# Kernel tuning notes

Hardware: AMD Instinct MI355X
Metric: run time of the kernel (lower is better)

Reference implementation:

```python
import jax, jax.numpy as jnp
import numpy as np

T, R, S, P, Rc = 100, 300, 500, 8, 50
DEATH_RATE = 0.02
LOG2PI = float(np.log(2.0 * np.pi))


def setup_inputs() -> dict:
    key = jax.random.key(0)
    ks = jax.random.split(key, 12)
    infections = jax.random.uniform(ks[0], (T, R, S)) * 1000.0 + 1.0
    case_rate_time = jax.random.uniform(ks[1], (T,)) * 0.5 + 0.1
    case_rate_region = jax.random.uniform(ks[2], (R,)) * 0.5 + 0.1
    Rs = jax.random.uniform(ks[3], (S,)) + 0.5
    Rtr = jax.random.uniform(ks[4], (T, R)) + 0.5
    transit_rate = jax.random.uniform(ks[5], (P,)) * 0.2 + 0.01
    transit_data = jax.random.uniform(ks[6], (R, R, P))  # nonnegative covariates
    case_data = jnp.floor(jax.random.uniform(ks[7], (T, R)) * 1000.0)
    death_data = jnp.floor(jax.random.uniform(ks[8], (T, R)) * 50.0)
    strain_data = jnp.floor(jax.random.uniform(ks[9], (T, Rc, S)) * 1.2)  # sparse counts
    mutation_matrix = jax.random.uniform(ks[10], (S, S)) * 0.1
    # each fine region assigned to one coarse region -> (Rc, R) 0/1 projection
    sample_matrix = jax.nn.one_hot(jnp.arange(R) % Rc, Rc, dtype=jnp.float32).T
    return dict(
        infections=infections,
        case_rate_time=case_rate_time,
        case_rate_region=case_rate_region,
        R0=jnp.float32(1.5),
        Rs=Rs,
        Rtr=Rtr,
        transit_rate=transit_rate,
        mutation_rate=jnp.float32(0.01),
        infection_od=jnp.float32(0.2),
        case_od=jnp.float32(0.2),
        death_od=jnp.float32(0.2),
        Rtr_drift_scale=jnp.float32(0.1),
        transit_data=transit_data,
        case_data=case_data,
        death_data=death_data,
        strain_data=strain_data,
        sample_matrix=sample_matrix,
        mutation_matrix=mutation_matrix,
    )


def _lognormal_lp(x, m, s):
    lx = jnp.log(x)
    return -lx - jnp.log(s) - 0.5 * LOG2PI - (lx - m) ** 2 / (2.0 * s * s)


def _negbin_lp(k, rate, od):
    # OverdispersedPoisson -> NegativeBinomial(r, p) with q=1/(1+od*rate)
    q = 1.0 / (1.0 + od * rate)
    p = 1.0 - q
    r = rate * q / p
    return (jax.lax.lgamma(k + r) - jax.lax.lgamma(r) - jax.lax.lgamma(k + 1.0)
            + r * jnp.log(q) + k * jnp.log(p))


def reference(infections, case_rate_time, case_rate_region, R0, Rs, Rtr,
              transit_rate, mutation_rate, infection_od, case_od, death_od,
              Rtr_drift_scale, transit_data, case_data, death_data,
              strain_data, sample_matrix, mutation_matrix):
    S_ = infections.shape[-1]
    Rtrs = R0 * Rs * Rtr[:, :, None]  # (T,R,S)
    mut = jnp.eye(S_, dtype=infections.dtype) + mutation_rate * mutation_matrix  # (S,S)
    transit = jnp.einsum('rRp,p->rR', transit_data, transit_rate)  # (R,R)
    # pred_infections = einsum('trs,trs,rRp,p,sS->tRS', prev, Rtrs[:-1], transit_data, transit_rate, mut)
    tmp = infections[:-1] * Rtrs[:-1]                    # (T-1,R,S)
    pred = jnp.einsum('trs,rR->tRs', tmp, transit)        # region mixing
    pred = jnp.einsum('tRs,sS->tRS', pred, mut)           # strain mutation mixing
    # torch clamps .data in-place -> straight-through gradient
    pred = pred + jax.lax.stop_gradient(jnp.maximum(pred, 1e-3) - pred)
    # RelaxedPoisson(pred, infection_od).log_prob(curr)
    s2 = jnp.log1p(1.0 / pred + infection_od)
    m = jnp.log(pred) - s2 / 2.0
    ll_step = _lognormal_lp(infections[1:], m, jnp.sqrt(s2)).sum()
    # Rtr_drift ~ LogNormal(0, Rtr_drift_scale), obs = Rtr[1:]/Rtr[:-1]
    ll_drift = _lognormal_lp(Rtr[1:] / Rtr[:-1], 0.0, Rtr_drift_scale).sum()
    # case / death observations (population=None)
    inf_sum = infections.sum(-1)                          # (T,R)
    case_rate = case_rate_time[:, None] * case_rate_region
    ll_case = _negbin_lp(case_data, inf_sum * case_rate, case_od).sum()
    ll_death = _negbin_lp(death_data, inf_sum * DEATH_RATE, death_od).sum()
    # strain multinomial (total_count does not enter log_prob; all-zero rows give 0)
    coarse = jnp.einsum('trs,Rr->tRs', infections, sample_matrix) + 1e-6
    logp = jnp.log(coarse) - jnp.log(coarse.sum(-1, keepdims=True))
    n = strain_data.sum(-1)
    ll_strain = (jax.lax.lgamma(n + 1.0)
                 - jax.lax.lgamma(strain_data + 1.0).sum(-1)
                 + (strain_data * logp).sum(-1)).sum()
    return ll_step + ll_drift + ll_case + ll_death + ll_strain
```

## Files before the change

kernel.cpp:

```cpp
#include <hip/hip_runtime.h>

#define T_   100
#define R_   300
#define S_   500
#define P_   8
#define RC_  50
#define TM1  99
#define TILE_I 8
#define NTILE 38
#define LOG2PI_F 1.8378770664093453f

#define RP   320
#define SPD  512
#define NTM  10

#define ACCS_OFF   0
#define FLAG_OFF   2048
#define SLV_OFF    2176
#define SLR_OFF    3776
#define SLN_OFF    5376
#define RSF_OFF    5632
#define RTRF_OFF   7680
#define TT_OFF     135680
#define MT_OFF     545280
#define XT_OFF     1069568
#define ROWSUM_OFF 33837568ull
#define WS_NEED    33957568ull
#define WB_OFF     33957568ull
#define WS_NEED2   54437568ull

#define NB_WB     50
#define NB_STR    1250
#define NB_XT     4000
#define NB_PA     528
#define NB_PMT    1024
#define NB_DR     117
#define NB_MEGA   (NB_WB + NB_STR + NB_XT + NB_PA + NB_PMT + NB_DR)
#define NB_CDB    118
#define NB_STEP   (TM1 * NTM + NB_CDB)

typedef __attribute__((ext_vector_type(8))) short s8v;
typedef __attribute__((ext_vector_type(4))) float f32x4;

static __device__ __forceinline__ float b2f(unsigned short h) {
    union { unsigned int u; float f; } v;
    v.u = ((unsigned int)h) << 16;
    return v.f;
}

static __device__ __forceinline__ unsigned short f2b(float f) {
    union { float f; unsigned int u; } v;
    v.f = f;
    unsigned int u = v.u;
    unsigned int r = u + 0x7FFFu + ((u >> 16) & 1u);
    return (unsigned short)(r >> 16);
}

template<bool BF>
static __device__ __forceinline__ float ld(const void* p, int i) {
    if (BF) return b2f(((const unsigned short*)p)[i]);
    return ((const float*)p)[i];
}

template<bool BF>
static __device__ __forceinline__ float2 ld2(const void* p, int i) {
    if (BF) {
        unsigned int u = *(const unsigned int*)((const unsigned short*)p + i);
        return make_float2(b2f((unsigned short)(u & 0xFFFFu)),
                           b2f((unsigned short)(u >> 16)));
    }
    return *(const float2*)((const float*)p + i);
}

static __device__ __forceinline__ float load_scalar(const void* vp) {
    const unsigned short* p = (const unsigned short*)vp;
    float b = b2f(p[0]);
    if (b > 0.004f && b < 4.1f) return b;
    return ((const float*)vp)[0];
}

static __device__ __forceinline__ void acc_add(float* accs, float v) {
    atomicAdd(accs + (blockIdx.x & 15) * 32, v);
}

__global__ void k_detect(const void* inf, const void* sm, float* accs, int* flag,
                         float* slV, int* slR, int* slN, int ws_ok, int ws_ok2) {
    const unsigned short* u = (const unsigned short*)inf;
    int ok = 1;
    for (int i = 0; i < 64; ++i) {
        float v = b2f(u[i]);
        if (!(v > 0.5f && v < 1300.0f)) ok = 0;
    }
    if (blockIdx.x == 0) {
        if (threadIdx.x < 16) accs[threadIdx.x * 32] = 0.0f;
        if (threadIdx.x == 0) {
            flag[0] = ok;
            flag[1] = ws_ok;
            flag[2] = ws_ok2;
        }
    }
    if (!ws_ok) return;
    int c = blockIdx.x;
    __shared__ int cl;
    if (threadIdx.x == 0) cl = 0;
    __syncthreads();
    for (int r = threadIdx.x; r < R_; r += 256) {
        float v = ok ? b2f(((const unsigned short*)sm)[c * R_ + r])
                     : ((const float*)sm)[c * R_ + r];
        if (v != 0.0f) {
            int k = atomicAdd(&cl, 1);
            if (k < 8) { slV[c * 8 + k] = v; slR[c * 8 + k] = r; }
        }
    }
    __syncthreads();
    if (threadIdx.x == 0) slN[c] = cl < 8 ? cl : 8;
}

static __device__ __forceinline__ float negbin_lp(float k, float rate, float od) {
    float q = 1.0f / (1.0f + od * rate);
    float p = 1.0f - q;
    float r = rate * q / p;
    return lgammaf(k + r) - lgammaf(r) - lgammaf(k + 1.0f)
         + r * __logf(q) + k * __logf(p);
}


template<bool BF>
static __device__ __forceinline__ void wb_blk(int vb, const void* td, const void* rate,
                                              const void* Rtr, const void* pR0,
                                              unsigned short* Wb) {
    int rowT = vb / 5;
    int rT   = vb - rowT * 5;
    int i0w = rowT * 32, r0 = rT * 64;
    int tid = threadIdx.x;
    int il = tid >> 3;
    int rgBase = r0 + (tid & 7) * 8;
    int ig = i0w + il;
    float R0 = load_scalar(pR0);
    float ratev[P_];
    #pragma unroll
    for (int p = 0; p < P_; ++p) ratev[p] = ld<BF>(rate, p);
    float tr[8];
    #pragma unroll
    for (int c = 0; c < 8; ++c) {
        int rg = rgBase + c;
        float s = 0.0f;
        if (rg < R_ && ig < R_) {
            #pragma unroll
            for (int p = 0; p < P_; ++p)
                s = fmaf(ld<BF>(td, (rg * R_ + ig) * P_ + p), ratev[p], s);
        }
        tr[c] = s * R0;
    }
    for (int t = 0; t < T_; ++t) {
        float rv[8];
        #pragma unroll
        for (int c2 = 0; c2 < 4; ++c2) {
            int rg = rgBase + c2 * 2;
            float2 v = (rg < R_) ? ld2<BF>(Rtr, t * R_ + rg) : make_float2(0.f, 0.f);
            rv[c2 * 2] = v.x; rv[c2 * 2 + 1] = v.y;
        }
        s8v o;
        #pragma unroll
        for (int c = 0; c < 8; ++c) o[c] = (short)f2b(tr[c] * rv[c]);
        *(s8v*)(Wb + ((size_t)(t * RP + ig)) * RP + rgBase) = o;
    }
}

template<bool BF>
static __device__ __forceinline__ void strain_blk(int vb, const void* inf,
                                                  const void* strain, const void* sm,
                                                  const float* slV, const int* slR,
                                                  const int* slN, int useList,
                                                  float* accs, char* smem) {
    int wave = threadIdx.x >> 6;
    int lane = threadIdx.x & 63;
    int id = vb * 4 + wave;
    int t = id / RC_;
    int c = id - t * RC_;
    int n;
    const float* wvP;
    const int*   wrP;
    int*   cnt4 = (int*)smem;
    float* wvL  = (float*)(smem + 16);
    int*   wrL  = (int*)(smem + 144);
    float* ws4  = (float*)(smem + 4096);
    if (useList) {
        n = slN[c];
        wvP = slV + c * 8;
        wrP = slR + c * 8;
    } else {
        if (threadIdx.x < 4) cnt4[threadIdx.x] = 0;
        __syncthreads();
        for (int base = 0; base < R_; base += 64) {
            int r = base + lane;
            float v = (r < R_) ? ld<BF>(sm, c * R_ + r) : 0.0f;
            if (v != 0.0f) {
                int k = atomicAdd(&cnt4[wave], 1);
                if (k < 8) { wvL[wave * 8 + k] = v; wrL[wave * 8 + k] = r; }
            }
        }
        __syncthreads();
        n = cnt4[wave] < 8 ? cnt4[wave] : 8;
        wvP = wvL + wave * 8;
        wrP = wrL + wave * 8;
    }

    float Plg = 0.0f, Pn = 0.0f, Ptot = 0.0f;
    int infBase = t * R_ * S_;
    int strBase = (t * RC_ + c) * S_;
    for (int it = 0; it < 4; ++it) {
        int s0 = it * 128 + lane * 2;
        if (s0 < S_) {
            float cx = 1e-6f, cy = 1e-6f;
            for (int k = 0; k < n; ++k) {
                float2 iv = ld2<BF>(inf, infBase + wrP[k] * S_ + s0);
                float wk = wvP[k];
                cx = fmaf(wk, iv.x, cx);
                cy = fmaf(wk, iv.y, cy);
            }
            float2 sd = ld2<BF>(strain, strBase + s0);
            Ptot += cx + cy;
            if (sd.x != 0.0f) {
                Plg += sd.x * __logf(cx);
                if (sd.x > 1.5f) Plg -= lgammaf(sd.x + 1.0f);
                Pn += sd.x;
            }
            if (sd.y != 0.0f) {
                Plg += sd.y * __logf(cy);
                if (sd.y > 1.5f) Plg -= lgammaf(sd.y + 1.0f);
                Pn += sd.y;
            }
        }
    }
    #pragma unroll
    for (int off = 32; off > 0; off >>= 1) {
        Plg  += __shfl_down(Plg,  off);
        Pn   += __shfl_down(Pn,   off);
        Ptot += __shfl_down(Ptot, off);
    }
    if (lane == 0)
        ws4[wave] = lgammaf(Pn + 1.0f) + Plg - Pn * __logf(Ptot);
    __syncthreads();
    if (threadIdx.x == 0)
        acc_add(accs, ws4[0] + ws4[1] + ws4[2] + ws4[3]);
}

template<bool BF>
static __device__ __forceinline__ void xt_blk(int vb, const void* inf,
                                              unsigned short* Xt, float* rowsum,
                                              char* smem) {
    unsigned short (*lds16)[66] = (unsigned short (*)[66])smem;
    int t   = vb / 40;
    int rem = vb - t * 40;
    int st  = rem / 5;
    int rt  = rem - st * 5;
    int s0 = st * 64, r0 = rt * 64;
    int tid = threadIdx.x;
    int j  = tid & 31;
    int i8 = tid >> 5;
    float rsum[8];
    #pragma unroll
    for (int p = 0; p < 8; ++p) {
        int rl = i8 + p * 8;
        int rr = r0 + rl;
        int ss = s0 + 2 * j;
        float2 v = (rr < R_ && ss < S_) ? ld2<BF>(inf, (t * R_ + rr) * S_ + ss)
                                        : make_float2(0.f, 0.f);
        lds16[2 * j][rl]     = f2b(v.x);
        lds16[2 * j + 1][rl] = f2b(v.y);
        rsum[p] = v.x + v.y;
    }
    __syncthreads();
    #pragma unroll
    for (int p = 0; p < 8; ++p) {
        int sl = i8 + p * 8;
        int ss = s0 + sl;
        unsigned int w = *(const unsigned int*)&lds16[sl][2 * j];
        *(unsigned int*)(Xt + ((size_t)(t * SPD + ss)) * RP + r0 + 2 * j) = w;
    }
    #pragma unroll
    for (int p = 0; p < 8; ++p) {
        float v = rsum[p];
        v += __shfl_xor(v, 1);  v += __shfl_xor(v, 2);  v += __shfl_xor(v, 4);
        v += __shfl_xor(v, 8);  v += __shfl_xor(v, 16);
        int rl = i8 + p * 8;
        if (j == 0 && r0 + rl < R_) atomicAdd(rowsum + t * R_ + r0 + rl, v);
    }
}

template<bool BF>
static __device__ __forceinline__ void prep_a_blk(int vb, const void* td, const void* rate,
                                                  const void* Rtr, const void* pR0,
                                                  const void* Rs, float* transitT,
                                                  float* RtrF, float* RsF) {
    int idx = vb * 256 + threadIdx.x;
    if (idx < RP * RP) {
        int i = idx / RP, r = idx - i * RP;
        float v = 0.0f;
        if (i < R_ && r < R_) {
            float s = 0.0f;
            #pragma unroll
            for (int p = 0; p < P_; ++p)
                s = fmaf(ld<BF>(td, (r * R_ + i) * P_ + p), ld<BF>(rate, p), s);
            v = s;
        }
        transitT[idx] = v;
    } else if (idx < RP * RP + T_ * RP) {
        int k = idx - RP * RP;
        int t = k / RP, r = k - t * RP;
        float v = 0.0f;
        if (r < R_) v = load_scalar(pR0) * ld<BF>(Rtr, t * R_ + r);
        RtrF[k] = v;
    } else if (idx < RP * RP + T_ * RP + SPD) {
        int s = idx - RP * RP - T_ * RP;
        RsF[s] = (s < S_) ? ld<BF>(Rs, s) : 0.0f;
    }
}

template<bool BF>
static __device__ __forceinline__ void prep_mt_blk(int vb, const void* mm,
                                                   unsigned short* Mt) {
    int idx = vb * 256 + threadIdx.x;
    int sp = idx >> 9, s = idx & (SPD - 1);
    float v = (s < S_ && sp < S_) ? ld<BF>(mm, s * S_ + sp) : 0.0f;
    Mt[idx] = f2b(v);
}

template<bool BF>
static __device__ __forceinline__ void drift_blk(int vb, const void* Rtr,
                                                 const void* pscale, float* accs,
                                                 char* smem) {
    float* ws4 = (float*)(smem + 4096);
    int wave = threadIdx.x >> 6;
    int lane = threadIdx.x & 63;
    int idx = vb * 256 + threadIdx.x;
    float v = 0.0f;
    if (idx < TM1 * R_) {
        int t = idx / R_;
        int r = idx - t * R_;
        float x  = ld<BF>(Rtr, (t + 1) * R_ + r) / ld<BF>(Rtr, t * R_ + r);
        float sc = load_scalar(pscale);
        float lx = __logf(x);
        v = -lx - __logf(sc) - 0.5f * LOG2PI_F - lx * lx / (2.0f * sc * sc);
    }
    #pragma unroll
    for (int off = 32; off > 0; off >>= 1) v += __shfl_down(v, off);
    if (lane == 0) ws4[wave] = v;
    __syncthreads();
    if (threadIdx.x == 0) acc_add(accs, ws4[0] + ws4[1] + ws4[2] + ws4[3]);
}

template<bool BF>
static __device__ __forceinline__ void mega_body(
        const void* inf, const void* strain, const void* sm,
        const void* td, const void* rate, const void* Rtr, const void* pR0,
        const void* Rs, const void* mm, const void* pdrift,
        float* transitT, float* RtrF, float* RsF, unsigned short* Mt,
        unsigned short* Xt, float* rowsum, unsigned short* Wb,
        const float* slV, const int* slR, const int* slN,
        const int* flag, float* accs, char* smem) {
    int bid = blockIdx.x;
    if (bid < NB_WB) {
        if (flag[2]) wb_blk<BF>(bid, td, rate, Rtr, pR0, Wb);
    } else if (bid < NB_WB + NB_STR) {
        strain_blk<BF>(bid - NB_WB, inf, strain, sm, slV, slR, slN, flag[1], accs, smem);
    } else if (bid < NB_WB + NB_STR + NB_XT) {
        if (flag[1]) xt_blk<BF>(bid - NB_WB - NB_STR, inf, Xt, rowsum, smem);
    } else if (bid < NB_WB + NB_STR + NB_XT + NB_PA) {
        if (flag[1]) prep_a_blk<BF>(bid - NB_WB - NB_STR - NB_XT, td, rate,
                                    Rtr, pR0, Rs, transitT, RtrF, RsF);
    } else if (bid < NB_WB + NB_STR + NB_XT + NB_PA + NB_PMT) {
        if (flag[1]) prep_mt_blk<BF>(bid - NB_WB - NB_STR - NB_XT - NB_PA, mm, Mt);
    } else {
        drift_blk<BF>(bid - NB_WB - NB_STR - NB_XT - NB_PA - NB_PMT, Rtr, pdrift,
                      accs, smem);
    }
}

__global__ void k_mega(
        const void* inf, const void* strain, const void* sm,
        const void* td, const void* rate, const void* Rtr, const void* pR0,
        const void* Rs, const void* mm, const void* pdrift,
        float* transitT, float* RtrF, float* RsF, unsigned short* Mt,
        unsigned short* Xt, float* rowsum, unsigned short* Wb,
        const float* slV, const int* slR, const int* slN,
        const int* flag, float* accs) {
    __shared__ __align__(16) char smem[8448];
    if (flag[0]) mega_body<true >(inf, strain, sm, td, rate, Rtr, pR0, Rs, mm, pdrift,
                                  transitT, RtrF, RsF, Mt, Xt, rowsum, Wb,
                                  slV, slR, slN, flag, accs, smem);
    else         mega_body<false>(inf, strain, sm, td, rate, Rtr, pR0, Rs, mm, pdrift,
                                  transitT, RtrF, RsF, Mt, Xt, rowsum, Wb,
                                  slV, slR, slN, flag, accs, smem);
}

template<bool BF>
static __device__ __forceinline__ void cdB_blk(int vb, const float* rowsum,
        const void* crt, const void* crr, const void* cased, const void* deathd,
        const void* pcod, const void* pdod, float* accs, float* sred) {
    int wave = threadIdx.x >> 6;
    int lane = threadIdx.x & 63;
    int row = vb * 256 + threadIdx.x;
    float v = 0.0f;
    if (row < T_ * R_) {
        int t = row / R_;
        int r = row - t * R_;
        float s = rowsum[row];
        v = negbin_lp(ld<BF>(cased, row),
                      s * ld<BF>(crt, t) * ld<BF>(crr, r), load_scalar(pcod))
          + negbin_lp(ld<BF>(deathd, row), s * 0.02f, load_scalar(pdod));
    }
    #pragma unroll
    for (int off = 32; off > 0; off >>= 1) v += __shfl_down(v, off);
    if (lane == 0) sred[wave] = v;
    __syncthreads();
    if (threadIdx.x == 0) acc_add(accs, sred[0] + sred[1] + sred[2] + sred[3]);
}

template<bool BF>
static __device__ __forceinline__ void mfma_step_body(
        const void* inf, const float* RsF, const float* RtrF, const float* transitT,
        const unsigned short* Mt, const unsigned short* Xt, const unsigned short* Wb,
        const void* pmr, const void* pod, const int* flag, float* accs,
        unsigned short* E_lds, float* sred) {
    const int nwg = TM1 * NTM;
    const int q = nwg >> 3, rm = nwg & 7;
    int bid = blockIdx.x;
    int xcd = bid & 7, ixc = bid >> 3;
    int wid = (xcd < rm) ? xcd * (q + 1) + ixc
                         : rm * (q + 1) + (xcd - rm) * q + ixc;
    int t    = wid / NTM;
    int tile = wid - t * NTM;
    int i0   = tile * 32;
    int tid  = threadIdx.x;
    int wave = tid >> 6, lane = tid & 63;
    int g    = lane >> 4, r15 = lane & 15;
    int colW = wave * 128;
    bool useWb = (flag[2] != 0);
    float mr = load_scalar(pmr);
    float od = load_scalar(pod);

    f32x4 c1[2][8];
    #pragma unroll
    for (int fr = 0; fr < 2; ++fr)
        #pragma unroll
        for (int fc = 0; fc < 8; ++fc)
            c1[fr][fc] = (f32x4){0.f, 0.f, 0.f, 0.f};

    const float* rrB = RtrF + t * RP;
    const unsigned short* xtB = Xt + (size_t)t * SPD * RP;
    const unsigned short* wbB = Wb + (size_t)t * RP * RP;
    for (int k = 0; k < RP / 32; ++k) {
        int ks = k * 32 + g * 8;
        s8v a[2];
        if (useWb) {
            a[0] = *(const s8v*)(wbB + (size_t)(i0 + r15) * RP + ks);
            a[1] = *(const s8v*)(wbB + (size_t)(i0 + 16 + r15) * RP + ks);
        } else {
            float4 rr0 = *(const float4*)(rrB + ks);
            float4 rr1 = *(const float4*)(rrB + ks + 4);
            #pragma unroll
            for (int fr = 0; fr < 2; ++fr) {
                int row = i0 + fr * 16 + r15;
                float4 t0 = *(const float4*)(transitT + row * RP + ks);
                float4 t1 = *(const float4*)(transitT + row * RP + ks + 4);
                a[fr][0] = (short)f2b(t0.x * rr0.x);
                a[fr][1] = (short)f2b(t0.y * rr0.y);
                a[fr][2] = (short)f2b(t0.z * rr0.z);
                a[fr][3] = (short)f2b(t0.w * rr0.w);
                a[fr][4] = (short)f2b(t1.x * rr1.x);
                a[fr][5] = (short)f2b(t1.y * rr1.y);
                a[fr][6] = (short)f2b(t1.z * rr1.z);
                a[fr][7] = (short)f2b(t1.w * rr1.w);
            }
        }
        #pragma unroll
        for (int fc = 0; fc < 8; ++fc) {
            int col = colW + fc * 16 + r15;
            s8v b = *(const s8v*)(xtB + (size_t)col * RP + ks);
            c1[0][fc] = __builtin_amdgcn_mfma_f32_16x16x32_bf16(a[0], b, c1[0][fc], 0, 0, 0);
            c1[1][fc] = __builtin_amdgcn_mfma_f32_16x16x32_bf16(a[1], b, c1[1][fc], 0, 0, 0);
        }
    }

    #pragma unroll
    for (int fc = 0; fc < 8; ++fc) {
        int col = colW + fc * 16 + r15;
        float rs = RsF[col];
        #pragma unroll
        for (int fr = 0; fr < 2; ++fr) {
            #pragma unroll
            for (int j = 0; j < 4; ++j) {
                int lrow = fr * 16 + g * 4 + j;
                int idx = (lrow * SPD + col) ^ ((lrow & 7) << 3);
                E_lds[idx] = f2b(c1[fr][fc][j] * rs);
            }
        }
    }
    __syncthreads();

    float myll = 0.0f;
    int swz = (r15 & 7) << 3;
    #pragma unroll
    for (int pass = 0; pass < 4; ++pass) {
        f32x4 c2[2][2];
        #pragma unroll
        for (int fr = 0; fr < 2; ++fr)
            #pragma unroll
            for (int fcx = 0; fcx < 2; ++fcx)
                c2[fr][fcx] = (f32x4){0.f, 0.f, 0.f, 0.f};
        #pragma unroll 2
        for (int k = 0; k < SPD / 32; ++k) {
            int ks = k * 32 + g * 8;
            s8v aE0 = *(const s8v*)(E_lds + ((r15 * SPD + ks) ^ swz));
            s8v aE1 = *(const s8v*)(E_lds + (((16 + r15) * SPD + ks) ^ swz));
            #pragma unroll
            for (int fcx = 0; fcx < 2; ++fcx) {
                int col = colW + (pass * 2 + fcx) * 16 + r15;
                s8v b = *(const s8v*)(Mt + col * SPD + ks);
                c2[0][fcx] = __builtin_amdgcn_mfma_f32_16x16x32_bf16(aE0, b, c2[0][fcx], 0, 0, 0);
                c2[1][fcx] = __builtin_amdgcn_mfma_f32_16x16x32_bf16(aE1, b, c2[1][fcx], 0, 0, 0);
            }
        }
        #pragma unroll
        for (int fcx = 0; fcx < 2; ++fcx) {
            int fc = pass * 2 + fcx;
            int col = colW + fc * 16 + r15;
            if (col < S_) {
                #pragma unroll
                for (int fr = 0; fr < 2; ++fr) {
                    #pragma unroll
                    for (int j = 0; j < 4; ++j) {
                        int lrow = fr * 16 + g * 4 + j;
                        int grow = i0 + lrow;
                        if (grow < R_) {
                            float e = b2f(E_lds[(lrow * SPD + col) ^ ((lrow & 7) << 3)]);
                            float pred = fmaf(mr, c2[fr][fcx][j], e);
                            pred = fmaxf(pred, 1e-3f);
                            float ip = __builtin_amdgcn_rcpf(pred);
                            float s2 = __logf(1.0f + ip + od);
                            float x  = ld<BF>(inf, ((t + 1) * R_ + grow) * S_ + col);
                            float lx = __logf(x);
                            float d  = lx - __logf(pred) + 0.5f * s2;
                            myll += -lx - 0.5f * __logf(s2) - 0.5f * LOG2PI_F
                                    - d * d * (0.5f * __builtin_amdgcn_rcpf(s2));
                        }
                    }
                }
            }
        }
    }
    #pragma unroll
    for (int off = 32; off > 0; off >>= 1) myll += __shfl_down(myll, off);
    if (lane == 0) sred[wave] = myll;
    __syncthreads();
    if (tid == 0) acc_add(accs, sred[0] + sred[1] + sred[2] + sred[3]);
}

__global__ void __launch_bounds__(256, 4)
TimeSpaceStrainModel_86397562126999_kernel(
        const void* inf, const float* RsF, const float* RtrF, const float* transitT,
        const unsigned short* Mt, const unsigned short* Xt, const unsigned short* Wb,
        const float* rowsum, const void* crt, const void* crr,
        const void* cased, const void* deathd, const void* pcod, const void* pdod,
        const void* pmr, const void* pod, const int* flag, float* accs) {
    __shared__ __align__(16) unsigned short E_lds[32 * SPD];
    __shared__ float sred[16];
    if (!flag[1]) return;
    if (blockIdx.x >= TM1 * NTM) {
        int vb = blockIdx.x - TM1 * NTM;
        if (flag[0]) cdB_blk<true >(vb, rowsum, crt, crr, cased, deathd, pcod, pdod, accs, sred);
        else         cdB_blk<false>(vb, rowsum, crt, crr, cased, deathd, pcod, pdod, accs, sred);
    } else {
        if (flag[0]) mfma_step_body<true >(inf, RsF, RtrF, transitT, Mt, Xt, Wb,
                                           pmr, pod, flag, accs, E_lds, sred);
        else         mfma_step_body<false>(inf, RsF, RtrF, transitT, Mt, Xt, Wb,
                                           pmr, pod, flag, accs, E_lds, sred);
    }
}

template<bool BF>
static __device__ __forceinline__ void casedeath_body(const void* inf, const void* crt,
                                                      const void* crr, const void* cased,
                                                      const void* deathd, const void* pcod,
                                                      const void* pdod, float* accs,
                                                      float* ws) {
    int wave = threadIdx.x >> 6;
    int lane = threadIdx.x & 63;
    int row  = blockIdx.x * 4 + wave;
    float s = 0.0f;
    if (row < T_ * R_) {
        int base = row * S_;
        for (int jj = lane; jj < S_ / 2; jj += 64) {
            float2 v = ld2<BF>(inf, base + 2 * jj);
            s += v.x + v.y;
        }
    }
    #pragma unroll
    for (int off = 32; off > 0; off >>= 1) s += __shfl_down(s, off);
    float v = 0.0f;
    if (lane == 0 && row < T_ * R_) {
        int t = row / R_;
        int r = row - t * R_;
        v = negbin_lp(ld<BF>(cased, row),
                      s * ld<BF>(crt, t) * ld<BF>(crr, r), load_scalar(pcod))
          + negbin_lp(ld<BF>(deathd, row), s * 0.02f, load_scalar(pdod));
    }
    if (lane == 0) ws[wave] = v;
    __syncthreads();
    if (threadIdx.x == 0) acc_add(accs, ws[0] + ws[1] + ws[2] + ws[3]);
}
__global__ void k_casedeath(const void* inf, const void* crt, const void* crr,
                            const void* cased, const void* deathd, const void* pcod,
                            const void* pdod, const int* flag, float* accs) {
    __shared__ float ws[4];
    if (flag[1]) return;
    if (flag[0]) casedeath_body<true>(inf, crt, crr, cased, deathd, pcod, pdod, accs, ws);
    else         casedeath_body<false>(inf, crt, crr, cased, deathd, pcod, pdod, accs, ws);
}

template<bool BF>
static __device__ __forceinline__ void step_body(const void* inf, const void* Rs,
                                                 const void* Rtr, const void* td,
                                                 const void* rate, const void* mm,
                                                 const void* pR0, const void* pmr,
                                                 const void* pod, float* accs,
                                                 float (*w)[TILE_I], float (*Et)[S_],
                                                 float* sred) {
    const int nwg = TM1 * NTILE;
    const int q = nwg >> 3, rr = nwg & 7;
    int bid = blockIdx.x;
    int xcd = bid & 7, ixc = bid >> 3;
    int wid = (xcd < rr) ? xcd * (q + 1) + ixc
                         : rr * (q + 1) + (xcd - rr) * q + ixc;
    int t    = wid / NTILE;
    int tile = wid - t * NTILE;
    int i0   = tile * TILE_I;
    int nrow = (R_ - i0) < TILE_I ? (R_ - i0) : TILE_I;
    int tid  = threadIdx.x;
    float R0 = load_scalar(pR0);
    float mr = load_scalar(pmr);
    float od = load_scalar(pod);

    {
        float ratev[P_];
        #pragma unroll
        for (int p = 0; p < P_; ++p) ratev[p] = ld<BF>(rate, p);
        for (int idx = tid; idx < R_ * TILE_I; idx += 256) {
            int r = idx >> 3;
            int i = idx & 7;
            float tv = 0.0f;
            if (i < nrow) {
                int tb = (r * R_ + i0 + i) * P_;
                #pragma unroll
                for (int p = 0; p < P_; ++p) tv = fmaf(ld<BF>(td, tb + p), ratev[p], tv);
            }
            w[r][i] = tv * ld<BF>(Rtr, t * R_ + r) * R0;
        }
    }
    __syncthreads();

    int c0 = tid * 2;
    bool on = (c0 < S_);
    int infBase = t * R_ * S_;

    float a0[TILE_I], a1[TILE_I];
    #pragma unroll
    for (int i = 0; i < TILE_I; ++i) { a0[i] = 0.0f; a1[i] = 0.0f; }
    #pragma unroll 2
    for (int r = 0; r < R_; ++r) {
        float2 x = on ? ld2<BF>(inf, infBase + r * S_ + c0) : make_float2(0.f, 0.f);
        float4 wa = *(const float4*)&w[r][0];
        float4 wb = *(const float4*)&w[r][4];
        a0[0] = fmaf(x.x, wa.x, a0[0]); a1[0] = fmaf(x.y, wa.x, a1[0]);
        a0[1] = fmaf(x.x, wa.y, a0[1]); a1[1] = fmaf(x.y, wa.y, a1[1]);
        a0[2] = fmaf(x.x, wa.z, a0[2]); a1[2] = fmaf(x.y, wa.z, a1[2]);
        a0[3] = fmaf(x.x, wa.w, a0[3]); a1[3] = fmaf(x.y, wa.w, a1[3]);
        a0[4] = fmaf(x.x, wb.x, a0[4]); a1[4] = fmaf(x.y, wb.x, a1[4]);
        a0[5] = fmaf(x.x, wb.y, a0[5]); a1[5] = fmaf(x.y, wb.y, a1[5]);
        a0[6] = fmaf(x.x, wb.z, a0[6]); a1[6] = fmaf(x.y, wb.z, a1[6]);
        a0[7] = fmaf(x.x, wb.w, a0[7]); a1[7] = fmaf(x.y, wb.w, a1[7]);
    }
    if (on) {
        float2 rs = ld2<BF>(Rs, c0);
        #pragma unroll
        for (int i = 0; i < TILE_I; ++i) {
            a0[i] *= rs.x;
            a1[i] *= rs.y;
            *(float2*)&Et[i][c0] = make_float2(a0[i], a1[i]);
        }
    }
    __syncthreads();

    float b0[TILE_I], b1[TILE_I];
    #pragma unroll
    for (int i = 0; i < TILE_I; ++i) { b0[i] = 0.0f; b1[i] = 0.0f; }
    for (int s = 0; s < S_; s += 4) {
        float2 m0, m1, m2, m3;
        if (on) {
            m0 = ld2<BF>(mm, (s    ) * S_ + c0);
            m1 = ld2<BF>(mm, (s + 1) * S_ + c0);
            m2 = ld2<BF>(mm, (s + 2) * S_ + c0);
            m3 = ld2<BF>(mm, (s + 3) * S_ + c0);
        } else {
            m0 = m1 = m2 = m3 = make_float2(0.f, 0.f);
        }
        #pragma unroll
        for (int i = 0; i < TILE_I; ++i) {
            float4 e = *(const float4*)&Et[i][s];
            b0[i] = fmaf(e.x, m0.x, b0[i]); b1[i] = fmaf(e.x, m0.y, b1[i]);
            b0[i] = fmaf(e.y, m1.x, b0[i]); b1[i] = fmaf(e.y, m1.y, b1[i]);
            b0[i] = fmaf(e.z, m2.x, b0[i]); b1[i] = fmaf(e.z, m2.y, b1[i]);
            b0[i] = fmaf(e.w, m3.x, b0[i]); b1[i] = fmaf(e.w, m3.y, b1[i]);
        }
    }

    float myll = 0.0f;
    if (on) {
        int infBase1 = (t + 1) * R_ * S_;
        #pragma unroll
        for (int i = 0; i < TILE_I; ++i) {
            if (i < nrow) {
                float2 x = ld2<BF>(inf, infBase1 + (i0 + i) * S_ + c0);
                {
                    float pred = a0[i] + mr * b0[i];
                    pred = pred > 1e-3f ? pred : 1e-3f;
                    float s2 = log1pf(1.0f / pred + od);
                    float mu = __logf(pred) - 0.5f * s2;
                    float lx = __logf(x.x);
                    float d  = lx - mu;
                    myll += -lx - 0.5f * __logf(s2) - 0.5f * LOG2PI_F
                            - d * d / (2.0f * s2);
                }
                {
                    float pred = a1[i] + mr * b1[i];
                    pred = pred > 1e-3f ? pred : 1e-3f;
                    float s2 = log1pf(1.0f / pred + od);
                    float mu = __logf(pred) - 0.5f * s2;
                    float lx = __logf(x.y);
                    float d  = lx - mu;
                    myll += -lx - 0.5f * __logf(s2) - 0.5f * LOG2PI_F
                            - d * d / (2.0f * s2);
                }
            }
        }
    }
    sred[tid] = myll;
    __syncthreads();
    for (int off = 128; off > 0; off >>= 1) {
        if (tid < off) sred[tid] += sred[tid + off];
        __syncthreads();
    }
    if (tid == 0) acc_add(accs, sred[0]);
}

__global__ void __launch_bounds__(256, 4)
k_step_valu(const void* inf, const void* Rs, const void* Rtr,
            const void* td, const void* rate, const void* mm,
            const void* pR0, const void* pmr, const void* pod,
            const int* flag, float* accs) {
    __shared__ float w[R_][TILE_I];
    __shared__ float Et[TILE_I][S_];
    __shared__ float sred[256];
    if (flag[1]) return;
    if (flag[0]) step_body<true >(inf, Rs, Rtr, td, rate, mm, pR0, pmr, pod, accs, w, Et, sred);
    else         step_body<false>(inf, Rs, Rtr, td, rate, mm, pR0, pmr, pod, accs, w, Et, sred);
}

__global__ void k_out(const float* accs, unsigned int* out) {
    if (threadIdx.x == 0 && blockIdx.x == 0) {
        float v = 0.0f;
        #pragma unroll
        for (int i = 0; i < 16; ++i) v += accs[i * 32];
        if (!(v == v)) v = -4.0e9f;
        else if (v > -1.0f && v < 1.0f) v = -2.0e9f;
        unsigned int b = (unsigned int)f2b(v);
        out[0] = (b << 16) | b;
    }
}

extern "C" void kernel_launch(void* const* d_in, const int* in_sizes, int n_in,
                              void* d_out, int out_size, void* d_ws, size_t ws_size,
                              hipStream_t stream) {
    const void* inf    = d_in[0];
    const void* crt    = d_in[1];
    const void* crr    = d_in[2];
    const void* pR0    = d_in[3];
    const void* Rs     = d_in[4];
    const void* Rtr    = d_in[5];
    const void* trate  = d_in[6];
    const void* pmr    = d_in[7];
    const void* piod   = d_in[8];
    const void* pcod   = d_in[9];
    const void* pdod   = d_in[10];
    const void* pdrift = d_in[11];
    const void* td     = d_in[12];
    const void* cased  = d_in[13];
    const void* deathd = d_in[14];
    const void* strain = d_in[15];
    const void* sm     = d_in[16];
    const void* mm     = d_in[17];

    char*  wsb  = (char*)d_ws;
    float* accs = (float*)(wsb + ACCS_OFF);
    int*   flag = (int*)(wsb + FLAG_OFF);
    float* slV      = (float*)(wsb + SLV_OFF);
    int*   slR      = (int*)(wsb + SLR_OFF);
    int*   slN      = (int*)(wsb + SLN_OFF);
    float* RsF      = (float*)(wsb + RSF_OFF);
    float* RtrF     = (float*)(wsb + RTRF_OFF);
    float* transitT = (float*)(wsb + TT_OFF);
    unsigned short* Mt = (unsigned short*)(wsb + MT_OFF);
    unsigned short* Xt = (unsigned short*)(wsb + XT_OFF);
    float* rowsum   = (float*)(wsb + ROWSUM_OFF);
    unsigned short* Wb = (unsigned short*)(wsb + WB_OFF);

    int ws_ok  = (ws_size >= WS_NEED)  ? 1 : 0;
    int ws_ok2 = (ws_size >= WS_NEED2) ? 1 : 0;

    if (ws_ok) hipMemsetAsync(rowsum, 0, T_ * R_ * sizeof(float), stream);
    k_detect<<<dim3(RC_), dim3(256), 0, stream>>>(inf, sm, accs, flag,
                                                  slV, slR, slN, ws_ok, ws_ok2);
    k_mega<<<dim3(NB_MEGA), dim3(256), 0, stream>>>(
        inf, strain, sm, td, trate, Rtr, pR0, Rs, mm, pdrift,
        transitT, RtrF, RsF, Mt, Xt, rowsum, Wb, slV, slR, slN, flag, accs);
    TimeSpaceStrainModel_86397562126999_kernel<<<dim3(NB_STEP), dim3(256), 0, stream>>>(
        inf, RsF, RtrF, transitT, Mt, Xt, Wb, rowsum, crt, crr,
        cased, deathd, pcod, pdod, pmr, piod, flag, accs);
    if (!ws_ok) {
        k_casedeath<<<dim3((T_ * R_ + 3) / 4), dim3(256), 0, stream>>>(
            inf, crt, crr, cased, deathd, pcod, pdod, flag, accs);
        k_step_valu<<<dim3(TM1 * NTILE), dim3(256), 0, stream>>>(
            inf, Rs, Rtr, td, trate, mm, pR0, pmr, piod, flag, accs);
    }
    k_out<<<dim3(1), dim3(64), 0, stream>>>(accs, (unsigned int*)d_out);
}
```

Before: 309.3 us.

## Pre-swizzle MFMA operands into fragment layout and move strain blocks into step kernel

Stores the Wb, Xt and Mt bf16 operand matrices in MFMA-fragment-major order, so each lane's 8-element operand load in the step kernel reads a contiguous 16-byte chunk. Mt is now built through an LDS transpose tile, which cuts its build from 1024 blocks to 64. When the sparse-list path is available, the strain-likelihood blocks move from the prep mega kernel into the step kernel to overlap with the MFMA work. prep_a skips building transitT when Wb is in use. The cost is more complex indexing and a larger step grid.

```diff
diff --git a/kernel.cpp b/kernel.cpp
--- a/kernel.cpp
+++ b/kernel.cpp
@@ -33,11 +33,11 @@
 #define NB_STR    1250
 #define NB_XT     4000
 #define NB_PA     528
-#define NB_PMT    1024
+#define NB_PMT    64
 #define NB_DR     117
 #define NB_MEGA   (NB_WB + NB_STR + NB_XT + NB_PA + NB_PMT + NB_DR)
 #define NB_CDB    118
-#define NB_STEP   (TM1 * NTM + NB_CDB)
+#define NB_STEP   (TM1 * NTM + NB_CDB + NB_STR)
 
 typedef __attribute__((ext_vector_type(8))) short s8v;
 typedef __attribute__((ext_vector_type(4))) float f32x4;
@@ -129,82 +129,67 @@
 static __device__ __forceinline__ void wb_blk(int vb, const void* td, const void* rate,
                                               const void* Rtr, const void* pR0,
                                               unsigned short* Wb) {
-    int rowT = vb / 5;
-    int rT   = vb - rowT * 5;
-    int i0w = rowT * 32, r0 = rT * 64;
-    int tid = threadIdx.x;
-    int il = tid >> 3;
-    int rgBase = r0 + (tid & 7) * 8;
-    int ig = i0w + il;
+    int rf2 = vb / 5, kT = vb - rf2 * 5;
+    int wv = threadIdx.x >> 6, l = threadIdx.x & 63;
+    int rf = rf2 * 2 + (wv >> 1);
+    int kg = kT * 2 + (wv & 1);
+    int i  = rf * 16 + (l & 15);
+    int rb = kg * 32 + (l >> 4) * 8;
     float R0 = load_scalar(pR0);
     float ratev[P_];
     #pragma unroll
     for (int p = 0; p < P_; ++p) ratev[p] = ld<BF>(rate, p);
     float tr[8];
     #pragma unroll
-    for (int c = 0; c < 8; ++c) {
-        int rg = rgBase + c;
+    for (int jj = 0; jj < 8; ++jj) {
+        int r = rb + jj;
         float s = 0.0f;
-        if (rg < R_ && ig < R_) {
+        if (r < R_ && i < R_) {
             #pragma unroll
             for (int p = 0; p < P_; ++p)
-                s = fmaf(ld<BF>(td, (rg * R_ + ig) * P_ + p), ratev[p], s);
-        }
-        tr[c] = s * R0;
+                s = fmaf(ld<BF>(td, (r * R_ + i) * P_ + p), ratev[p], s);
+        }
+        tr[jj] = s * R0;
     }
     for (int t = 0; t < T_; ++t) {
-        float rv[8];
-        #pragma unroll
-        for (int c2 = 0; c2 < 4; ++c2) {
-            int rg = rgBase + c2 * 2;
-            float2 v = (rg < R_) ? ld2<BF>(Rtr, t * R_ + rg) : make_float2(0.f, 0.f);
-            rv[c2 * 2] = v.x; rv[c2 * 2 + 1] = v.y;
-        }
         s8v o;
         #pragma unroll
-        for (int c = 0; c < 8; ++c) o[c] = (short)f2b(tr[c] * rv[c]);
-        *(s8v*)(Wb + ((size_t)(t * RP + ig)) * RP + rgBase) = o;
+        for (int jj = 0; jj < 8; ++jj) {
+            int r = rb + jj;
+            float rv = (r < R_) ? ld<BF>(Rtr, t * R_ + r) : 0.0f;
+            o[jj] = (short)f2b(tr[jj] * rv);
+        }
+        *(s8v*)(Wb + ((((size_t)t * 20 + rf) * 10 + kg) * 64 + l) * 8) = o;
     }
 }
 
 template<bool BF>
 static __device__ __forceinline__ void strain_blk(int vb, const void* inf,
                                                   const void* strain, const void* sm,
-                                                  const float* slV, const int* slR,
-                                                  const int* slN, int useList,
                                                   float* accs, char* smem) {
     int wave = threadIdx.x >> 6;
     int lane = threadIdx.x & 63;
     int id = vb * 4 + wave;
     int t = id / RC_;
     int c = id - t * RC_;
-    int n;
-    const float* wvP;
-    const int*   wrP;
     int*   cnt4 = (int*)smem;
     float* wvL  = (float*)(smem + 16);
     int*   wrL  = (int*)(smem + 144);
     float* ws4  = (float*)(smem + 4096);
-    if (useList) {
-        n = slN[c];
-        wvP = slV + c * 8;
-        wrP = slR + c * 8;
-    } else {
-        if (threadIdx.x < 4) cnt4[threadIdx.x] = 0;
-        __syncthreads();
-        for (int base = 0; base < R_; base += 64) {
-            int r = base + lane;
-            float v = (r < R_) ? ld<BF>(sm, c * R_ + r) : 0.0f;
-            if (v != 0.0f) {
-                int k = atomicAdd(&cnt4[wave], 1);
-                if (k < 8) { wvL[wave * 8 + k] = v; wrL[wave * 8 + k] = r; }
-            }
-        }
-        __syncthreads();
-        n = cnt4[wave] < 8 ? cnt4[wave] : 8;
-        wvP = wvL + wave * 8;
-        wrP = wrL + wave * 8;
-    }
+    if (threadIdx.x < 4) cnt4[threadIdx.x] = 0;
+    __syncthreads();
+    for (int base = 0; base < R_; base += 64) {
+        int r = base + lane;
+        float v = (r < R_) ? ld<BF>(sm, c * R_ + r) : 0.0f;
+        if (v != 0.0f) {
+            int k = atomicAdd(&cnt4[wave], 1);
+            if (k < 8) { wvL[wave * 8 + k] = v; wrL[wave * 8 + k] = r; }
+        }
+    }
+    __syncthreads();
+    int n = cnt4[wave] < 8 ? cnt4[wave] : 8;
+    const float* wvP = wvL + wave * 8;
+    const int*   wrP = wrL + wave * 8;
 
     float Plg = 0.0f, Pn = 0.0f, Ptot = 0.0f;
     int infBase = t * R_ * S_;
@@ -250,7 +235,7 @@
 static __device__ __forceinline__ void xt_blk(int vb, const void* inf,
                                               unsigned short* Xt, float* rowsum,
                                               char* smem) {
-    unsigned short (*lds16)[66] = (unsigned short (*)[66])smem;
+    unsigned short (*lds)[72] = (unsigned short (*)[72])smem;
     int t   = vb / 40;
     int rem = vb - t * 40;
     int st  = rem / 5;
@@ -267,17 +252,22 @@
         int ss = s0 + 2 * j;
         float2 v = (rr < R_ && ss < S_) ? ld2<BF>(inf, (t * R_ + rr) * S_ + ss)
                                         : make_float2(0.f, 0.f);
-        lds16[2 * j][rl]     = f2b(v.x);
-        lds16[2 * j + 1][rl] = f2b(v.y);
+        lds[2 * j][rl]     = f2b(v.x);
+        lds[2 * j + 1][rl] = f2b(v.y);
         rsum[p] = v.x + v.y;
     }
     __syncthreads();
-    #pragma unroll
-    for (int p = 0; p < 8; ++p) {
-        int sl = i8 + p * 8;
-        int ss = s0 + sl;
-        unsigned int w = *(const unsigned int*)&lds16[sl][2 * j];
-        *(unsigned int*)(Xt + ((size_t)(t * SPD + ss)) * RP + r0 + 2 * j) = w;
+    int l = tid & 63, w = tid >> 6;
+    #pragma unroll
+    for (int p = 0; p < 2; ++p) {
+        int fi  = p * 4 + w;
+        int ctl = fi >> 1, kl = fi & 1;
+        int sl  = ctl * 16 + (l & 15);
+        int rl  = kl * 32 + (l >> 4) * 8;
+        s8v vv = *(const s8v*)&lds[sl][rl];
+        int ct_g = st * 4 + ctl;
+        int k_g  = rt * 2 + kl;
+        *(s8v*)(Xt + ((((size_t)t * 32 + ct_g) * 10 + k_g) * 64 + l) * 8) = vv;
     }
     #pragma unroll
     for (int p = 0; p < 8; ++p) {
@@ -293,9 +283,10 @@
 static __device__ __forceinline__ void prep_a_blk(int vb, const void* td, const void* rate,
                                                   const void* Rtr, const void* pR0,
                                                   const void* Rs, float* transitT,
-                                                  float* RtrF, float* RsF) {
+                                                  float* RtrF, float* RsF, int flag2) {
     int idx = vb * 256 + threadIdx.x;
     if (idx < RP * RP) {
+        if (flag2) return;
         int i = idx / RP, r = idx - i * RP;
         float v = 0.0f;
         if (i < R_ && r < R_) {
@@ -319,12 +310,38 @@
 }
 
 template<bool BF>
-static __device__ __forceinline__ void prep_mt_blk(int vb, const void* mm,
-                                                   unsigned short* Mt) {
-    int idx = vb * 256 + threadIdx.x;
-    int sp = idx >> 9, s = idx & (SPD - 1);
-    float v = (s < S_ && sp < S_) ? ld<BF>(mm, s * S_ + sp) : 0.0f;
-    Mt[idx] = f2b(v);
+static __device__ __forceinline__ void mt_blk(int vb, const void* mm,
+                                              unsigned short* Mt, char* smem) {
+    unsigned short (*lds)[72] = (unsigned short (*)[72])smem;
+    int spT = vb >> 3;
+    int sT  = vb & 7;
+    int sp0 = spT * 64, ss0 = sT * 64;
+    int tid = threadIdx.x;
+    int j  = tid & 31;
+    int i8 = tid >> 5;
+    #pragma unroll
+    for (int p = 0; p < 8; ++p) {
+        int sl = i8 + p * 8;
+        int s  = ss0 + sl;
+        int sp = sp0 + 2 * j;
+        float2 v = (s < S_ && sp < S_) ? ld2<BF>(mm, s * S_ + sp)
+                                       : make_float2(0.f, 0.f);
+        lds[2 * j][sl]     = f2b(v.x);
+        lds[2 * j + 1][sl] = f2b(v.y);
+    }
+    __syncthreads();
+    int l = tid & 63, w = tid >> 6;
+    #pragma unroll
+    for (int p = 0; p < 2; ++p) {
+        int fi  = p * 4 + w;
+        int ctl = fi >> 1, kl = fi & 1;
+        int spl = ctl * 16 + (l & 15);
+        int sll = kl * 32 + (l >> 4) * 8;
+        s8v vv = *(const s8v*)&lds[spl][sll];
+        int ct_g = spT * 4 + ctl;
+        int k_g  = sT * 2 + kl;
+        *(s8v*)(Mt + (((size_t)ct_g * 16 + k_g) * 64 + l) * 8) = vv;
+    }
 }
 
 template<bool BF>
@@ -358,20 +375,19 @@
         const void* Rs, const void* mm, const void* pdrift,
         float* transitT, float* RtrF, float* RsF, unsigned short* Mt,
         unsigned short* Xt, float* rowsum, unsigned short* Wb,
-        const float* slV, const int* slR, const int* slN,
         const int* flag, float* accs, char* smem) {
     int bid = blockIdx.x;
     if (bid < NB_WB) {
         if (flag[2]) wb_blk<BF>(bid, td, rate, Rtr, pR0, Wb);
     } else if (bid < NB_WB + NB_STR) {
-        strain_blk<BF>(bid - NB_WB, inf, strain, sm, slV, slR, slN, flag[1], accs, smem);
+        if (!flag[1]) strain_blk<BF>(bid - NB_WB, inf, strain, sm, accs, smem);
     } else if (bid < NB_WB + NB_STR + NB_XT) {
         if (flag[1]) xt_blk<BF>(bid - NB_WB - NB_STR, inf, Xt, rowsum, smem);
     } else if (bid < NB_WB + NB_STR + NB_XT + NB_PA) {
         if (flag[1]) prep_a_blk<BF>(bid - NB_WB - NB_STR - NB_XT, td, rate,
-                                    Rtr, pR0, Rs, transitT, RtrF, RsF);
+                                    Rtr, pR0, Rs, transitT, RtrF, RsF, flag[2]);
     } else if (bid < NB_WB + NB_STR + NB_XT + NB_PA + NB_PMT) {
-        if (flag[1]) prep_mt_blk<BF>(bid - NB_WB - NB_STR - NB_XT - NB_PA, mm, Mt);
+        if (flag[1]) mt_blk<BF>(bid - NB_WB - NB_STR - NB_XT - NB_PA, mm, Mt, smem);
     } else {
         drift_blk<BF>(bid - NB_WB - NB_STR - NB_XT - NB_PA - NB_PMT, Rtr, pdrift,
                       accs, smem);
@@ -384,15 +400,12 @@
         const void* Rs, const void* mm, const void* pdrift,
         float* transitT, float* RtrF, float* RsF, unsigned short* Mt,
         unsigned short* Xt, float* rowsum, unsigned short* Wb,
-        const float* slV, const int* slR, const int* slN,
         const int* flag, float* accs) {
-    __shared__ __align__(16) char smem[8448];
+    __shared__ __align__(16) char smem[9728];
     if (flag[0]) mega_body<true >(inf, strain, sm, td, rate, Rtr, pR0, Rs, mm, pdrift,
-                                  transitT, RtrF, RsF, Mt, Xt, rowsum, Wb,
-                                  slV, slR, slN, flag, accs, smem);
+                                  transitT, RtrF, RsF, Mt, Xt, rowsum, Wb, flag, accs, smem);
     else         mega_body<false>(inf, strain, sm, td, rate, Rtr, pR0, Rs, mm, pdrift,
-                                  transitT, RtrF, RsF, Mt, Xt, rowsum, Wb,
-                                  slV, slR, slN, flag, accs, smem);
+                                  transitT, RtrF, RsF, Mt, Xt, rowsum, Wb, flag, accs, smem);
 }
 
 template<bool BF>
@@ -416,6 +429,59 @@
     if (lane == 0) sred[wave] = v;
     __syncthreads();
     if (threadIdx.x == 0) acc_add(accs, sred[0] + sred[1] + sred[2] + sred[3]);
+}
+
+template<bool BF>
+static __device__ __forceinline__ void strainL_blk(int vb, const void* inf,
+        const void* strain, const float* slV, const int* slR, const int* slN,
+        float* accs, float* ws4) {
+    int wave = threadIdx.x >> 6;
+    int lane = threadIdx.x & 63;
+    int id = vb * 4 + wave;
+    int t = id / RC_;
+    int c = id - t * RC_;
+    int n = slN[c];
+    const float* wvP = slV + c * 8;
+    const int*   wrP = slR + c * 8;
+
+    float Plg = 0.0f, Pn = 0.0f, Ptot = 0.0f;
+    int infBase = t * R_ * S_;
+    int strBase = (t * RC_ + c) * S_;
+    for (int it = 0; it < 4; ++it) {
+        int s0 = it * 128 + lane * 2;
+        if (s0 < S_) {
+            float cx = 1e-6f, cy = 1e-6f;
+            for (int k = 0; k < n; ++k) {
+                float2 iv = ld2<BF>(inf, infBase + wrP[k] * S_ + s0);
+                float wk = wvP[k];
+                cx = fmaf(wk, iv.x, cx);
+                cy = fmaf(wk, iv.y, cy);
+            }
+            float2 sd = ld2<BF>(strain, strBase + s0);
+            Ptot += cx + cy;
+            if (sd.x != 0.0f) {
+                Plg += sd.x * __logf(cx);
+                if (sd.x > 1.5f) Plg -= lgammaf(sd.x + 1.0f);
+                Pn += sd.x;
+            }
+            if (sd.y != 0.0f) {
+                Plg += sd.y * __logf(cy);
+                if (sd.y > 1.5f) Plg -= lgammaf(sd.y + 1.0f);
+                Pn += sd.y;
+            }
+        }
+    }
+    #pragma unroll
+    for (int off = 32; off > 0; off >>= 1) {
+        Plg  += __shfl_down(Plg,  off);
+        Pn   += __shfl_down(Pn,   off);
+        Ptot += __shfl_down(Ptot, off);
+    }
+    if (lane == 0)
+        ws4[wave] = lgammaf(Pn + 1.0f) + Plg - Pn * __logf(Ptot);
+    __syncthreads();
+    if (threadIdx.x == 0)
+        acc_add(accs, ws4[0] + ws4[1] + ws4[2] + ws4[3]);
 }
 
 template<bool BF>
@@ -437,6 +503,7 @@
     int wave = tid >> 6, lane = tid & 63;
     int g    = lane >> 4, r15 = lane & 15;
     int colW = wave * 128;
+    int ct0  = colW >> 4;
     bool useWb = (flag[2] != 0);
     float mr = load_scalar(pmr);
     float od = load_scalar(pod);
@@ -449,15 +516,16 @@
             c1[fr][fc] = (f32x4){0.f, 0.f, 0.f, 0.f};
 
     const float* rrB = RtrF + t * RP;
-    const unsigned short* xtB = Xt + (size_t)t * SPD * RP;
-    const unsigned short* wbB = Wb + (size_t)t * RP * RP;
+    const unsigned short* xtB = Xt + (size_t)t * 32 * 10 * 512;
+    const unsigned short* wbB = Wb + (size_t)t * 20 * 10 * 512;
+    int rf0 = i0 >> 4;
     for (int k = 0; k < RP / 32; ++k) {
-        int ks = k * 32 + g * 8;
         s8v a[2];
         if (useWb) {
-            a[0] = *(const s8v*)(wbB + (size_t)(i0 + r15) * RP + ks);
-            a[1] = *(const s8v*)(wbB + (size_t)(i0 + 16 + r15) * RP + ks);
+            a[0] = *(const s8v*)(wbB + (((size_t)(rf0    ) * 10 + k) * 64 + lane) * 8);
+            a[1] = *(const s8v*)(wbB + (((size_t)(rf0 + 1) * 10 + k) * 64 + lane) * 8);
         } else {
+            int ks = k * 32 + g * 8;
             float4 rr0 = *(const float4*)(rrB + ks);
             float4 rr1 = *(const float4*)(rrB + ks + 4);
             #pragma unroll
@@ -477,8 +545,7 @@
         }
         #pragma unroll
         for (int fc = 0; fc < 8; ++fc) {
-            int col = colW + fc * 16 + r15;
-            s8v b = *(const s8v*)(xtB + (size_t)col * RP + ks);
+            s8v b = *(const s8v*)(xtB + (((size_t)(ct0 + fc) * 10 + k) * 64 + lane) * 8);
             c1[0][fc] = __builtin_amdgcn_mfma_f32_16x16x32_bf16(a[0], b, c1[0][fc], 0, 0, 0);
             c1[1][fc] = __builtin_amdgcn_mfma_f32_16x16x32_bf16(a[1], b, c1[1][fc], 0, 0, 0);
         }
@@ -517,8 +584,8 @@
             s8v aE1 = *(const s8v*)(E_lds + (((16 + r15) * SPD + ks) ^ swz));
             #pragma unroll
             for (int fcx = 0; fcx < 2; ++fcx) {
-                int col = colW + (pass * 2 + fcx) * 16 + r15;
-                s8v b = *(const s8v*)(Mt + col * SPD + ks);
+                int ct = ct0 + pass * 2 + fcx;
+                s8v b = *(const s8v*)(Mt + (((size_t)ct * 16 + k) * 64 + lane) * 8);
                 c2[0][fcx] = __builtin_amdgcn_mfma_f32_16x16x32_bf16(aE0, b, c2[0][fcx], 0, 0, 0);
                 c2[1][fcx] = __builtin_amdgcn_mfma_f32_16x16x32_bf16(aE1, b, c2[1][fcx], 0, 0, 0);
             }
@@ -564,12 +631,19 @@
         const unsigned short* Mt, const unsigned short* Xt, const unsigned short* Wb,
         const float* rowsum, const void* crt, const void* crr,
         const void* cased, const void* deathd, const void* pcod, const void* pdod,
-        const void* pmr, const void* pod, const int* flag, float* accs) {
+        const void* pmr, const void* pod, const void* strain,
+        const float* slV, const int* slR, const int* slN,
+        const int* flag, float* accs) {
     __shared__ __align__(16) unsigned short E_lds[32 * SPD];
     __shared__ float sred[16];
     if (!flag[1]) return;
-    if (blockIdx.x >= TM1 * NTM) {
-        int vb = blockIdx.x - TM1 * NTM;
+    int bid = blockIdx.x;
+    if (bid >= TM1 * NTM + NB_CDB) {
+        int vb = bid - TM1 * NTM - NB_CDB;
+        if (flag[0]) strainL_blk<true >(vb, inf, strain, slV, slR, slN, accs, sred);
+        else         strainL_blk<false>(vb, inf, strain, slV, slR, slN, accs, sred);
+    } else if (bid >= TM1 * NTM) {
+        int vb = bid - TM1 * NTM;
         if (flag[0]) cdB_blk<true >(vb, rowsum, crt, crr, cased, deathd, pcod, pdod, accs, sred);
         else         cdB_blk<false>(vb, rowsum, crt, crr, cased, deathd, pcod, pdod, accs, sred);
     } else {
@@ -824,10 +898,10 @@
                                                   slV, slR, slN, ws_ok, ws_ok2);
     k_mega<<<dim3(NB_MEGA), dim3(256), 0, stream>>>(
         inf, strain, sm, td, trate, Rtr, pR0, Rs, mm, pdrift,
-        transitT, RtrF, RsF, Mt, Xt, rowsum, Wb, slV, slR, slN, flag, accs);
+        transitT, RtrF, RsF, Mt, Xt, rowsum, Wb, flag, accs);
     TimeSpaceStrainModel_86397562126999_kernel<<<dim3(NB_STEP), dim3(256), 0, stream>>>(
         inf, RsF, RtrF, transitT, Mt, Xt, Wb, rowsum, crt, crr,
-        cased, deathd, pcod, pdod, pmr, piod, flag, accs);
+        cased, deathd, pcod, pdod, pmr, piod, strain, slV, slR, slN, flag, accs);
     if (!ws_ok) {
         k_casedeath<<<dim3((T_ * R_ + 3) / 4), dim3(256), 0, stream>>>(
             inf, crt, crr, cased, deathd, pcod, pdod, flag, accs);
```

New measurement: 273.3 us. 1.13x faster.
